# Performance work log

Measured on AMD Instinct MI355X. Metric: run time of the kernel, lower is better.

## Reference

```python
import jax, jax.numpy as jnp
import numpy as np

HIDDEN = 3072
N_HEADS = 24
N_KV = 8
HEAD_DIM = HIDDEN // N_HEADS          # 128
ROT = int(HEAD_DIM * 0.75)            # 96 (partial rotary)
OP_SIZE = N_HEADS * HEAD_DIM + 2 * N_KV * HEAD_DIM  # 5120
LORA_R = 256
LORA_SCALE = 512.0 / LORA_R           # 2.0
ROPE_THETA = 10000.0
SCALE = HEAD_DIM ** -0.5


def setup_inputs() -> dict:
    key = jax.random.key(0)
    ks = jax.random.split(key, 8)
    B, S = 2, 2048
    hidden_states = jax.random.normal(ks[0], (B, S, HIDDEN), dtype=jnp.float32)
    position_ids = jnp.arange(B * S, dtype=jnp.int64 if jax.config.jax_enable_x64 else jnp.int32).reshape(B, S)
    w = lambda k, o, i: jax.random.normal(k, (o, i), dtype=jnp.float32) * (i ** -0.5)
    return {
        "hidden_states": hidden_states,
        "Wqkv": w(ks[1], OP_SIZE, HIDDEN),
        "Aqkv": w(ks[2], LORA_R, HIDDEN),
        "Bqkv": w(ks[3], OP_SIZE, LORA_R) * 0.01,
        "Wo": w(ks[4], HIDDEN, N_HEADS * HEAD_DIM),
        "Ao": w(ks[5], LORA_R, N_HEADS * HEAD_DIM),
        "Bo": w(ks[6], HIDDEN, LORA_R) * 0.01,
        "position_ids": position_ids,
    }


def _lora_linear(x, W, A, Bm):
    # base GEMM + low-rank LoRA update, scaling = alpha/r
    return x @ W.T + (x @ A.T) @ Bm.T * LORA_SCALE


def _rotate_half(x):
    h = x.shape[-1] // 2
    return jnp.concatenate((-x[..., h:], x[..., :h]), axis=-1)


def reference(hidden_states, Wqkv, Aqkv, Bqkv, Wo, Ao, Bo, position_ids):
    B, S, _ = hidden_states.shape
    qkv = _lora_linear(hidden_states, Wqkv, Aqkv, Bqkv)  # [B,S,5120]
    q_pos = N_HEADS * HEAD_DIM
    kv_pos = N_KV * HEAD_DIM
    q = qkv[..., :q_pos].reshape(B, S, N_HEADS, HEAD_DIM)
    k = qkv[..., q_pos:q_pos + kv_pos].reshape(B, S, N_KV, HEAD_DIM)
    v = qkv[..., q_pos + kv_pos:].reshape(B, S, N_KV, HEAD_DIM)

    # partial RoPE: cos/sin cache over rotary_ndims=96
    inv_freq = 1.0 / (ROPE_THETA ** (jnp.arange(0, ROT, 2, dtype=jnp.float32) / ROT))  # [48]
    freqs = position_ids.astype(jnp.float32)[..., None] * inv_freq  # [B,S,48]
    emb = jnp.concatenate((freqs, freqs), axis=-1)                   # [B,S,96]
    cos = jnp.cos(emb)[:, :, None, :]  # broadcast over head axis (bsnd)
    sin = jnp.sin(emb)[:, :, None, :]

    def rope(x):
        xr, xp = x[..., :ROT], x[..., ROT:]
        xr = xr * cos + _rotate_half(xr) * sin
        return jnp.concatenate((xr, xp), axis=-1)

    q = rope(q)
    k = rope(k)

    # GQA: repeat kv heads to match query heads
    groups = N_HEADS // N_KV
    k = jnp.repeat(k, groups, axis=2)
    v = jnp.repeat(v, groups, axis=2)

    scores = jnp.einsum('bqhd,bkhd->bhqk', q, k) * SCALE  # [B,H,S,S]
    causal = jnp.tril(jnp.ones((S, S), dtype=bool))
    scores = jnp.where(causal, scores, jnp.finfo(scores.dtype).min)
    probs = jax.nn.softmax(scores, axis=-1)
    attn = jnp.einsum('bhqk,bkhd->bqhd', probs, v).reshape(B, S, N_HEADS * HEAD_DIM)
    return _lora_linear(attn, Wo, Ao, Bo)
```

## Files before the change

kernel.cpp:

```cpp
#include <hip/hip_runtime.h>

typedef unsigned short u16;
typedef unsigned int   u32;

typedef __bf16 bf16_t;
typedef bf16_t bf16x8 __attribute__((ext_vector_type(8)));
typedef float  f32x4  __attribute__((ext_vector_type(4)));
typedef float  f32x16 __attribute__((ext_vector_type(16)));
typedef u16    u16x8  __attribute__((ext_vector_type(8)));
typedef u32    u32x4  __attribute__((ext_vector_type(4)));

__device__ __forceinline__ float bf2f(u16 u) { return __uint_as_float(((u32)u) << 16); }
__device__ __forceinline__ u16 f2bf(float f) {
  u32 u = __float_as_uint(f);
  u32 r = u + 0x7fffu + ((u >> 16) & 1u);
  return (u16)(r >> 16);
}
__device__ __forceinline__ float fast_exp2(float x) { return __builtin_amdgcn_exp2f(x); }

__device__ __forceinline__ void gload_lds16(const u16* g, u16* l) {
  __builtin_amdgcn_global_load_lds(
      (const __attribute__((address_space(1))) void*)g,
      (__attribute__((address_space(3))) void*)l,
      16, 0, 0);
}

#define SBAR0() __builtin_amdgcn_sched_barrier(0)
#define HWBAR() __builtin_amdgcn_s_barrier()

__global__ void k_cast_all(const float* __restrict__ x,  const float* __restrict__ wq,
                           const float* __restrict__ bq, const float* __restrict__ aq,
                           const float* __restrict__ wo, const float* __restrict__ bo,
                           const float* __restrict__ ao,
                           u16* __restrict__ xw, u16* __restrict__ wwq, u16* __restrict__ aqkvb,
                           u16* __restrict__ wwo, u16* __restrict__ aob) {
  const int total = 5177344;
  int i = blockIdx.x * blockDim.x + threadIdx.x;
  const int stride = gridDim.x * blockDim.x;
  for (; i < total; i += stride) {
    const float* src; u16* dst; int r, c8, L, off, sL;
    if (i < 1572864)      { int loc = i;           r = loc / 384; c8 = loc - r * 384; src = x;  dst = xw;    L = 3328; off = 0;    sL = 3072; }
    else if (i < 3538944) { int loc = i - 1572864; r = loc / 384; c8 = loc - r * 384; src = wq; dst = wwq;   L = 3328; off = 0;    sL = 3072; }
    else if (i < 3702784) { int loc = i - 3538944; r = loc >> 5;  c8 = loc & 31;      src = bq; dst = wwq;   L = 3328; off = 3072; sL = 256;  }
    else if (i < 3801088) { int loc = i - 3702784; r = loc / 384; c8 = loc - r * 384; src = aq; dst = aqkvb; L = 3072; off = 0;    sL = 3072; }
    else if (i < 4980736) { int loc = i - 3801088; r = loc / 384; c8 = loc - r * 384; src = wo; dst = wwo;   L = 3328; off = 0;    sL = 3072; }
    else if (i < 5079040) { int loc = i - 4980736; r = loc >> 5;  c8 = loc & 31;      src = bo; dst = wwo;   L = 3328; off = 3072; sL = 256;  }
    else                  { int loc = i - 5079040; r = loc / 384; c8 = loc - r * 384; src = ao; dst = aob;   L = 3072; off = 0;    sL = 3072; }
    const f32x4* p = (const f32x4*)(src + (size_t)r * sL + c8 * 8);
    f32x4 a = p[0], b2 = p[1];
    u16x8 o;
    o[0] = f2bf(a[0]);  o[1] = f2bf(a[1]);  o[2] = f2bf(a[2]);  o[3] = f2bf(a[3]);
    o[4] = f2bf(b2[0]); o[5] = f2bf(b2[1]); o[6] = f2bf(b2[2]); o[7] = f2bf(b2[3]);
    *(u16x8*)(dst + (size_t)r * L + off + c8 * 8) = o;
  }
}

__global__ void k_red4_cast(const float* __restrict__ t4, u16* __restrict__ out,
                            int C8, int L, int off, float scale, size_t plane) {
  const int r  = blockIdx.y;
  const int c8 = blockIdx.x * 64 + threadIdx.x;
  if (c8 >= C8) return;
  size_t base = (size_t)r * (C8 * 8) + c8 * 8;
  float s[8];
#pragma unroll
  for (int j = 0; j < 8; ++j) s[j] = 0.f;
#pragma unroll
  for (int p = 0; p < 4; ++p) {
    const f32x4* q = (const f32x4*)(t4 + p * plane + base);
    f32x4 a = q[0], b = q[1];
    s[0] += a[0]; s[1] += a[1]; s[2] += a[2]; s[3] += a[3];
    s[4] += b[0]; s[5] += b[1]; s[6] += b[2]; s[7] += b[3];
  }
  u16x8 o;
#pragma unroll
  for (int j = 0; j < 8; ++j) o[j] = f2bf(s[j] * scale);
  *(u16x8*)(out + (size_t)r * L + off + c8 * 8) = o;
}

__global__ __launch_bounds__(256) void k_gemm_bt_sk(
    const u16* __restrict__ A, const u16* __restrict__ B, float* __restrict__ C,
    int M, int N, int lda, int ldb, int kc) {
  __shared__ u16 As[64][64 + 8];
  __shared__ u16 Bs[64][64 + 8];
  const int tid   = threadIdx.x;
  const int lane  = tid & 63;
  const int w     = tid >> 6;
  const int wm    = (w >> 1) * 32;
  const int wn    = (w & 1) * 32;
  const int row16 = lane & 15;
  const int quad  = lane >> 4;
  const int m0 = blockIdx.y * 64;
  const int n0 = blockIdx.x * 64;
  const int ldr = tid >> 2;
  const int ldc = (tid & 3) * 16;
  const int z   = blockIdx.z;
  float* Cz = C + (size_t)z * M * N;
  const int kbeg = z * kc, kend = kbeg + kc;

  f32x4 acc[2][2] = {};

  for (int k0 = kbeg; k0 < kend; k0 += 64) {
    const u16* ga = A + (size_t)(m0 + ldr) * lda + (k0 + ldc);
    const u16* gb = B + (size_t)(n0 + ldr) * ldb + (k0 + ldc);
    u16x8 a0 = *(const u16x8*)ga;
    u16x8 a1 = *(const u16x8*)(ga + 8);
    u16x8 b0 = *(const u16x8*)gb;
    u16x8 b1 = *(const u16x8*)(gb + 8);
    __syncthreads();
    *(u16x8*)&As[ldr][ldc]     = a0;
    *(u16x8*)&As[ldr][ldc + 8] = a1;
    *(u16x8*)&Bs[ldr][ldc]     = b0;
    *(u16x8*)&Bs[ldr][ldc + 8] = b1;
    __syncthreads();
#pragma unroll
    for (int kk = 0; kk < 64; kk += 32) {
      bf16x8 af0 = *(const bf16x8*)&As[wm + row16][kk + quad * 8];
      bf16x8 af1 = *(const bf16x8*)&As[wm + 16 + row16][kk + quad * 8];
      bf16x8 bg0 = *(const bf16x8*)&Bs[wn + row16][kk + quad * 8];
      bf16x8 bg1 = *(const bf16x8*)&Bs[wn + 16 + row16][kk + quad * 8];
      acc[0][0] = __builtin_amdgcn_mfma_f32_16x16x32_bf16(af0, bg0, acc[0][0], 0, 0, 0);
      acc[0][1] = __builtin_amdgcn_mfma_f32_16x16x32_bf16(af0, bg1, acc[0][1], 0, 0, 0);
      acc[1][0] = __builtin_amdgcn_mfma_f32_16x16x32_bf16(af1, bg0, acc[1][0], 0, 0, 0);
      acc[1][1] = __builtin_amdgcn_mfma_f32_16x16x32_bf16(af1, bg1, acc[1][1], 0, 0, 0);
    }
  }
#pragma unroll
  for (int tm = 0; tm < 2; ++tm)
#pragma unroll
    for (int tn = 0; tn < 2; ++tn) {
      int gm = m0 + wm + tm * 16 + quad * 4;
      int gn = n0 + wn + tn * 16 + row16;
#pragma unroll
      for (int r = 0; r < 4; ++r)
        Cz[(size_t)(gm + r) * N + gn] = acc[tm][tn][r];
    }
}

__device__ __forceinline__ void stage_half(
    int H, int nt4,
    const u16* __restrict__ A, const u16* __restrict__ B, int K,
    int m0, int n0, u16* AsB, u16* BsB,
    int w, int rowin, int colsw) {
  if (H >= nt4) return;
  const int t = H >> 2, slot = H & 3;
  const int half = slot & 1;
  const u16* G = (slot < 2) ? A : B;
  const int r0 = (slot < 2) ? m0 : n0;
  u16* lds = ((slot < 2) ? AsB : BsB) + (t & 1) * 16384 + half * 8192;
  const int k0 = t * 64;
#pragma unroll
  for (int i = 0; i < 2; ++i) {
    const int chunk = w * 2 + i;
    const int row = half * 128 + chunk * 8 + rowin;
    gload_lds16(G + (size_t)(r0 + row) * K + k0 + colsw, lds + chunk * 512);
  }
}

__device__ __forceinline__ bf16x8 frag_ld(const u16* base, int row, int c16) {
  return *(const bf16x8*)(base + row * 64 + ((c16 ^ (row & 7)) << 3));
}

template <int RB>
__device__ __forceinline__ void gemm256_group(
    int k, int nt,
    const u16* __restrict__ A, const u16* __restrict__ B, int K,
    int m0, int n0, u16* AsB, u16* BsB,
    int wr, int wc, int row16, int quad, int w, int rowin, int colsw,
    f32x4 (&acc)[8][4]) {
  const u16* Ab = AsB + RB * 16384;
  const u16* Bb = BsB + RB * 16384;
  const int nt4 = nt * 4;
  bf16x8 a0[4][2], a1[4][2], b0[2][2], b1[2][2];

#pragma unroll
  for (int mf = 0; mf < 4; ++mf)
#pragma unroll
    for (int kk = 0; kk < 2; ++kk)
      a0[mf][kk] = frag_ld(Ab, wr * 128 + mf * 16 + row16, kk * 4 + quad);
#pragma unroll
  for (int nf = 0; nf < 2; ++nf)
#pragma unroll
    for (int kk = 0; kk < 2; ++kk)
      b0[nf][kk] = frag_ld(Bb, wc * 64 + nf * 16 + row16, kk * 4 + quad);
  stage_half(4 * k + 5, nt4, A, B, K, m0, n0, AsB, BsB, w, rowin, colsw);
  SBAR0(); HWBAR(); SBAR0();
  __builtin_amdgcn_s_setprio(1);
#pragma unroll
  for (int mf = 0; mf < 4; ++mf)
#pragma unroll
    for (int nf = 0; nf < 2; ++nf)
#pragma unroll
      for (int kk = 0; kk < 2; ++kk)
        acc[mf][nf] = __builtin_amdgcn_mfma_f32_16x16x32_bf16(a0[mf][kk], b0[nf][kk], acc[mf][nf], 0, 0, 0);
  __builtin_amdgcn_s_setprio(0);
  SBAR0(); HWBAR(); SBAR0();

#pragma unroll
  for (int nf = 0; nf < 2; ++nf)
#pragma unroll
    for (int kk = 0; kk < 2; ++kk)
      b1[nf][kk] = frag_ld(Bb, wc * 64 + 32 + nf * 16 + row16, kk * 4 + quad);
  stage_half(4 * k + 6, nt4, A, B, K, m0, n0, AsB, BsB, w, rowin, colsw);
  SBAR0(); HWBAR(); SBAR0();
  __builtin_amdgcn_s_setprio(1);
#pragma unroll
  for (int mf = 0; mf < 4; ++mf)
#pragma unroll
    for (int nf = 0; nf < 2; ++nf)
#pragma unroll
      for (int kk = 0; kk < 2; ++kk)
        acc[mf][2 + nf] = __builtin_amdgcn_mfma_f32_16x16x32_bf16(a0[mf][kk], b1[nf][kk], acc[mf][2 + nf], 0, 0, 0);
  __builtin_amdgcn_s_setprio(0);
  SBAR0(); HWBAR(); SBAR0();

#pragma unroll
  for (int mf = 0; mf < 4; ++mf)
#pragma unroll
    for (int kk = 0; kk < 2; ++kk)
      a1[mf][kk] = frag_ld(Ab, wr * 128 + 64 + mf * 16 + row16, kk * 4 + quad);
  stage_half(4 * k + 7, nt4, A, B, K, m0, n0, AsB, BsB, w, rowin, colsw);
  SBAR0(); HWBAR(); SBAR0();
  __builtin_amdgcn_s_setprio(1);
#pragma unroll
  for (int mf = 0; mf < 4; ++mf)
#pragma unroll
    for (int nf = 0; nf < 2; ++nf)
#pragma unroll
      for (int kk = 0; kk < 2; ++kk)
        acc[4 + mf][nf] = __builtin_amdgcn_mfma_f32_16x16x32_bf16(a1[mf][kk], b0[nf][kk], acc[4 + mf][nf], 0, 0, 0);
  __builtin_amdgcn_s_setprio(0);
  SBAR0(); HWBAR(); SBAR0();

  stage_half(4 * k + 8, nt4, A, B, K, m0, n0, AsB, BsB, w, rowin, colsw);
  SBAR0();
  if (k < nt - 2) { asm volatile("s_waitcnt vmcnt(2)" ::: "memory"); }
  else            { asm volatile("s_waitcnt vmcnt(0)" ::: "memory"); }
  HWBAR(); SBAR0();
  __builtin_amdgcn_s_setprio(1);
#pragma unroll
  for (int mf = 0; mf < 4; ++mf)
#pragma unroll
    for (int nf = 0; nf < 2; ++nf)
#pragma unroll
      for (int kk = 0; kk < 2; ++kk)
        acc[4 + mf][2 + nf] = __builtin_amdgcn_mfma_f32_16x16x32_bf16(a1[mf][kk], b1[nf][kk], acc[4 + mf][2 + nf], 0, 0, 0);
  __builtin_amdgcn_s_setprio(0);
  SBAR0(); HWBAR(); SBAR0();
}

__global__ __launch_bounds__(512, 2) void k_gemm256(
    const u16* __restrict__ A, const u16* __restrict__ B, float* __restrict__ C,
    int M, int N, int K) {
  __shared__ u16 As[2 * 16384];
  __shared__ u16 Bs[2 * 16384];

  const int tid   = threadIdx.x;
  const int lane  = tid & 63;
  const int w     = tid >> 6;
  const int wr    = w >> 2;
  const int wc    = w & 3;
  const int row16 = lane & 15;
  const int quad  = lane >> 4;
  const int rowin = lane >> 3;
  const int colsw = ((lane & 7) ^ (lane >> 3)) << 3;

  const int nwg = (int)gridDim.x;
  const int bid = (int)blockIdx.x;
  const int xcd = bid & 7, rest = bid >> 3;
  const int qq = nwg >> 3, rr = nwg & 7;
  const int wg = (xcd < rr ? xcd * (qq + 1) : rr * (qq + 1) + (xcd - rr) * qq) + rest;
  const int nbx = N >> 8;
  const int m0 = (wg / nbx) << 8;
  const int n0 = (wg % nbx) << 8;

  const int nt = K >> 6;
  f32x4 acc[8][4] = {};

#pragma unroll
  for (int H = 0; H < 5; ++H)
    stage_half(H, nt * 4, A, B, K, m0, n0, As, Bs, w, rowin, colsw);
  asm volatile("s_waitcnt vmcnt(2)" ::: "memory");
  HWBAR(); SBAR0();

  int k = 0;
  for (; k + 1 < nt; k += 2) {
    gemm256_group<0>(k,     nt, A, B, K, m0, n0, As, Bs, wr, wc, row16, quad, w, rowin, colsw, acc);
    gemm256_group<1>(k + 1, nt, A, B, K, m0, n0, As, Bs, wr, wc, row16, quad, w, rowin, colsw, acc);
  }
  if (k < nt)
    gemm256_group<0>(k, nt, A, B, K, m0, n0, As, Bs, wr, wc, row16, quad, w, rowin, colsw, acc);

#pragma unroll
  for (int mi = 0; mi < 8; ++mi) {
    const int gm = m0 + wr * 128 + mi * 16 + quad * 4;
#pragma unroll
    for (int nj = 0; nj < 4; ++nj) {
      const int gn = n0 + wc * 64 + nj * 16 + row16;
#pragma unroll
      for (int r = 0; r < 4; ++r)
        C[(size_t)(gm + r) * N + gn] = acc[mi][nj][r];
    }
  }
}

__global__ void k_rope_tab(const int* __restrict__ pos_ids, float* __restrict__ tab,
                           int* __restrict__ ctr) {
  if (blockIdx.x == 0 && threadIdx.x == 0) *ctr = 0;
  const int t = threadIdx.x;
  const int r = blockIdx.x * 4 + t / 48;
  const int j = t % 48;
  const float pos = (float)pos_ids[r];
  float invf = powf(10000.0f, -(float)j * (1.0f / 48.0f));
  float e = pos * invf;
  tab[(size_t)r * 96 + j]      = cosf(e);
  tab[(size_t)r * 96 + 48 + j] = sinf(e);
}

__global__ void k_rope_v(const float* __restrict__ qkv, const float* __restrict__ tab,
                         u16* __restrict__ qb, u16* __restrict__ kb, u16* __restrict__ vtg) {
  const int y = blockIdx.y;
  const int d = threadIdx.x;
  if (y < 32) {
    const int r  = blockIdx.x;
    const int hh = y;
    const float* src;
    if (hh < 24) src = qkv + (size_t)r * 5120 + hh * 128;
    else         src = qkv + (size_t)r * 5120 + 3072 + (hh - 24) * 128;
    float x = src[d];
    float outv;
    if (d >= 96) {
      outv = x;
    } else {
      int j = (d < 48) ? d : d - 48;
      float c  = tab[(size_t)r * 96 + j];
      float sn = tab[(size_t)r * 96 + 48 + j];
      if (d < 48) outv = x * c - src[d + 48] * sn;
      else        outv = x * c + src[d - 48] * sn;
    }
    u16 o = f2bf(outv);
    if (hh < 24) qb[((size_t)r * 24 + hh) * 128 + d] = o;
    else         kb[((size_t)r * 8 + (hh - 24)) * 128 + d] = o;
  } else {
    const int bk = blockIdx.x >> 8;
    const int kg = blockIdx.x & 255;
    const int b = bk >> 3, kvh = bk & 7;
    const float* src = qkv + (size_t)(b * 2048 + kg * 8) * 5120 + 4096 + kvh * 128 + d;
    u16x8 pack;
#pragma unroll
    for (int t = 0; t < 8; ++t) pack[t] = f2bf(src[(size_t)t * 5120]);
    *(u16x8*)(vtg + ((size_t)bk * 128 + d) * 2048 + kg * 8) = pack;
  }
}

#define NJOBS 768

__global__ __launch_bounds__(256) void k_attn_mfma(
    const u16* __restrict__ qb, const u16* __restrict__ kb, const u16* __restrict__ vtg,
    u16* __restrict__ attnw, int* __restrict__ ctr) {
  __shared__ u16 Ks0[8192], Ks1[8192];
  __shared__ u16 Vt0[8192], Vt1[8192];
  __shared__ int s_job;

  const int tid  = threadIdx.x;
  const int lane = tid & 63;
  const int w    = tid >> 6;
  const int l31  = lane & 31;
  const int hi   = lane >> 5;
  const int r7   = lane & 7;
  const float C1 = 0.08838834764831845f * 1.4426950408889634f;

  for (;;) {
    if (tid == 0) s_job = atomicAdd(ctr, 1);
    __syncthreads();
    const int j = s_job;
    if (j >= NJOBS) return;

    const int qt  = 15 - (j / 48);
    const int bh  = j % 48;
    const int b   = bh / 24;
    const int h   = bh % 24;
    const int kvh = h / 3;
    const int q0  = qt * 128;
    const int qrow = q0 + w * 32 + l31;

    const u16* qrb = qb + (((size_t)(b * 2048 + qrow)) * 24 + h) * 128;
    bf16x8 qf[8];
#pragma unroll
    for (int kk = 0; kk < 8; ++kk) qf[kk] = *(const bf16x8*)(qrb + kk * 16 + hi * 8);

    const u16* kbbase = kb + ((size_t)(b * 2048) * 8 + kvh) * 128;
    const u16* vtbase = vtg + (size_t)(b * 8 + kvh) * 128 * 2048;

    f32x16 o32[4] = {};
    float m_st = -INFINITY, l_st = 0.f;
    const int ntile = 2 * qt + 2;

#define STAGE_K(Kd, KB0)                                                        \
  { _Pragma("unroll") for (int i = 0; i < 4; ++i) {                             \
      const int c = w * 4 + i;                                                  \
      const int rowk = 4 * c + (lane >> 4);                                     \
      gload_lds16(kbbase + (size_t)((KB0) + rowk) * 1024 +                      \
                      (((lane & 15) ^ (rowk & 7)) << 3),                        \
                  (Kd) + c * 512); } }
#define STAGE_V(Vd, KB0)                                                        \
  { _Pragma("unroll") for (int i = 0; i < 4; ++i) {                             \
      const int c = w * 4 + i;                                                  \
      const int rowv = 8 * c + (lane >> 3);                                     \
      gload_lds16(vtbase + (size_t)rowv * 2048 + (KB0) +                        \
                      (((lane & 7) ^ (rowv & 7)) << 3),                         \
                  (Vd) + c * 512); } }

    STAGE_K(Ks0, 0);
    STAGE_V(Vt0, 0);

    for (int t = 0; t < ntile; ++t) {
      const int kb0 = t * 64;
      const u16* Kc = (t & 1) ? Ks1 : Ks0;
      const u16* Vc = (t & 1) ? Vt1 : Vt0;

      asm volatile("s_waitcnt vmcnt(0)" ::: "memory");
      SBAR0(); HWBAR(); SBAR0();
      if (t + 1 < ntile) {
        u16* Kn = (t & 1) ? Ks0 : Ks1;
        u16* Vn = (t & 1) ? Vt0 : Vt1;
        STAGE_K(Kn, kb0 + 64);
        STAGE_V(Vn, kb0 + 64);
      }
      SBAR0();

      f32x16 s0 = {}, s1 = {};
      __builtin_amdgcn_s_setprio(1);
#pragma unroll
      for (int kk = 0; kk < 8; ++kk) {
        bf16x8 kf0 = *(const bf16x8*)&Kc[l31 * 128 + (((2 * kk + hi) ^ r7) << 3)];
        s0 = __builtin_amdgcn_mfma_f32_32x32x16_bf16(kf0, qf[kk], s0, 0, 0, 0);
        bf16x8 kf1 = *(const bf16x8*)&Kc[(32 + l31) * 128 + (((2 * kk + hi) ^ ((32 + l31) & 7)) << 3)];
        s1 = __builtin_amdgcn_mfma_f32_32x32x16_bf16(kf1, qf[kk], s1, 0, 0, 0);
      }
      __builtin_amdgcn_s_setprio(0);

      if (kb0 >= q0) {
#pragma unroll
        for (int r = 0; r < 16; ++r) {
          const int crow = (r & 3) + 8 * (r >> 2) + 4 * hi;
          if (kb0 + crow > qrow)      s0[r] = -INFINITY;
          if (kb0 + 32 + crow > qrow) s1[r] = -INFINITY;
        }
      }

      float tm[8];
#pragma unroll
      for (int r = 0; r < 8; ++r)
        tm[r] = fmaxf(fmaxf(s0[r], s0[r + 8]), fmaxf(s1[r], s1[r + 8]));
#pragma unroll
      for (int st = 4; st >= 1; st >>= 1)
#pragma unroll
        for (int r = 0; r < 4; ++r)
          if (r < st) tm[r] = fmaxf(tm[r], tm[r + st]);
      float mx = fmaxf(tm[0], __shfl_xor(tm[0], 32));

      const bool skip = __all((mx - m_st) * C1 <= 8.0f);
      if (!skip) {
        const float mnew = fmaxf(m_st, mx);
        const float alpha = fast_exp2((m_st - mnew) * C1);
        l_st *= alpha;
#pragma unroll
        for (int dt = 0; dt < 4; ++dt)
#pragma unroll
          for (int r = 0; r < 16; ++r) o32[dt][r] *= alpha;
        m_st = mnew;
      }
      const float mc = m_st * C1;
      float ts[8];
#pragma unroll
      for (int r = 0; r < 16; ++r) {
        s0[r] = fast_exp2(__builtin_fmaf(s0[r], C1, -mc));
        s1[r] = fast_exp2(__builtin_fmaf(s1[r], C1, -mc));
      }
#pragma unroll
      for (int r = 0; r < 8; ++r) ts[r] = (s0[r] + s0[r + 8]) + (s1[r] + s1[r + 8]);
#pragma unroll
      for (int st = 4; st >= 1; st >>= 1)
#pragma unroll
        for (int r = 0; r < 4; ++r)
          if (r < st) ts[r] += ts[r + st];
      l_st += ts[0] + __shfl_xor(ts[0], 32);

#pragma unroll
      for (int kt = 0; kt < 2; ++kt) {
        const f32x16& sv = kt ? s1 : s0;
        u32 pk[8];
#pragma unroll
        for (int i = 0; i < 8; ++i)
          asm("v_cvt_pk_bf16_f32 %0, %1, %2"
              : "=v"(pk[i]) : "v"(sv[2 * i]), "v"(sv[2 * i + 1]));
        u32 e0 = __shfl_xor(hi ? pk[0] : pk[2], 32);
        u32 e1 = __shfl_xor(hi ? pk[1] : pk[3], 32);
        u32 e2 = __shfl_xor(hi ? pk[4] : pk[6], 32);
        u32 e3 = __shfl_xor(hi ? pk[5] : pk[7], 32);
        u32x4 w0, w1;
        w0[0] = hi ? e0 : pk[0]; w0[1] = hi ? e1 : pk[1];
        w0[2] = hi ? pk[2] : e0; w0[3] = hi ? pk[3] : e1;
        w1[0] = hi ? e2 : pk[4]; w1[1] = hi ? e3 : pk[5];
        w1[2] = hi ? pk[6] : e2; w1[3] = hi ? pk[7] : e3;
        bf16x8 pb0 = __builtin_bit_cast(bf16x8, w0);
        bf16x8 pb1 = __builtin_bit_cast(bf16x8, w1);
        __builtin_amdgcn_s_setprio(1);
#pragma unroll
        for (int dt = 0; dt < 4; ++dt) {
          const int vrow = dt * 32 + l31;
          bf16x8 vf0 = *(const bf16x8*)&Vc[vrow * 64 + (((2 * (2 * kt) + hi) ^ (vrow & 7)) << 3)];
          o32[dt] = __builtin_amdgcn_mfma_f32_32x32x16_bf16(vf0, pb0, o32[dt], 0, 0, 0);
          bf16x8 vf1 = *(const bf16x8*)&Vc[vrow * 64 + (((2 * (2 * kt + 1) + hi) ^ (vrow & 7)) << 3)];
          o32[dt] = __builtin_amdgcn_mfma_f32_32x32x16_bf16(vf1, pb1, o32[dt], 0, 0, 0);
        }
        __builtin_amdgcn_s_setprio(0);
      }
    }

    __syncthreads();
    const float inv = 1.0f / l_st;
    u16* scr = ((w < 2) ? Ks0 : Ks1) + (w & 1) * 4096;
#pragma unroll
    for (int dt = 0; dt < 4; ++dt)
#pragma unroll
      for (int r = 0; r < 16; ++r) {
        const int d = 32 * dt + (r & 3) + 8 * (r >> 2) + 4 * hi;
        const int slot = (d >> 3) ^ (l31 & 7);
        scr[l31 * 128 + slot * 8 + (d & 7)] = f2bf(o32[dt][r] * inv);
      }
    const int q32r = lane >> 1, part = lane & 1;
    const size_t grow = ((size_t)(b * 2048 + q0 + w * 32 + q32r)) * 3328 + (size_t)h * 128;
#pragma unroll
    for (int c = 0; c < 8; ++c) {
      const int d0 = part * 64 + c * 8;
      const int s2 = (d0 >> 3) ^ (q32r & 7);
      *(u16x8*)(attnw + grow + d0) = *(const u16x8*)&scr[q32r * 128 + s2 * 8];
    }
  }
}

#define OFF_XW    ((size_t)0)
#define OFF_WWQ   ((size_t)27262976)
#define OFF_AQKVB ((size_t)61341696)
#define OFF_WWO   ((size_t)62914560)
#define OFF_AOB   ((size_t)83361792)
#define OFF_QKV   ((size_t)84934656)
#define OFF_TA4   OFF_QKV
#define OFF_QB    OFF_XW
#define OFF_KB    OFF_WWQ
#define OFF_VTG   (OFF_WWQ + (size_t)8388608)
#define OFF_RTAB  (OFF_WWQ + (size_t)16777216)
#define OFF_CTR   (OFF_WWQ + (size_t)18350080)
#define OFF_ATTNW OFF_QKV
#define OFF_TO4   (OFF_QKV + (size_t)27262976)

extern "C" void kernel_launch(void* const* d_in, const int* in_sizes, int n_in,
                              void* d_out, int out_size, void* d_ws, size_t ws_size,
                              hipStream_t stream) {
  const float* x    = (const float*)d_in[0];
  const float* Wqkv = (const float*)d_in[1];
  const float* Aqkv = (const float*)d_in[2];
  const float* Bqkv = (const float*)d_in[3];
  const float* Wo   = (const float*)d_in[4];
  const float* Ao   = (const float*)d_in[5];
  const float* Bo   = (const float*)d_in[6];
  const int*   pos  = (const int*)d_in[7];
  float* out = (float*)d_out;
  char* ws = (char*)d_ws;

  u16* xw    = (u16*)(ws + OFF_XW);
  u16* wwq   = (u16*)(ws + OFF_WWQ);
  u16* aqkvb = (u16*)(ws + OFF_AQKVB);
  u16* wwo   = (u16*)(ws + OFF_WWO);
  u16* aob   = (u16*)(ws + OFF_AOB);
  float* qkv = (float*)(ws + OFF_QKV);
  float* tA4 = (float*)(ws + OFF_TA4);
  u16* qb    = (u16*)(ws + OFF_QB);
  u16* kb    = (u16*)(ws + OFF_KB);
  u16* vtg   = (u16*)(ws + OFF_VTG);
  float* rtab = (float*)(ws + OFF_RTAB);
  int* ctr   = (int*)(ws + OFF_CTR);
  u16* attnw = (u16*)(ws + OFF_ATTNW);
  float* tO4 = (float*)(ws + OFF_TO4);

  k_cast_all<<<2048, 256, 0, stream>>>(x, Wqkv, Bqkv, Aqkv, Wo, Bo, Ao,
                                       xw, wwq, aqkvb, wwo, aob);

  k_gemm_bt_sk<<<dim3(4, 64, 4), 256, 0, stream>>>(xw, aqkvb, tA4, 4096, 256, 3328, 3072, 768);
  k_red4_cast<<<dim3(1, 4096), 64, 0, stream>>>(tA4, xw, 32, 3328, 3072, 2.f, (size_t)4096 * 256);

  k_gemm256<<<dim3((5120 / 256) * (4096 / 256)), 512, 0, stream>>>(xw, wwq, qkv, 4096, 5120, 3328);

  k_rope_tab<<<dim3(1024), 192, 0, stream>>>(pos, rtab, ctr);
  k_rope_v<<<dim3(4096, 33), 128, 0, stream>>>(qkv, rtab, qb, kb, vtg);

  k_attn_mfma<<<dim3(512), 256, 0, stream>>>(qb, kb, vtg, attnw, ctr);

  k_gemm_bt_sk<<<dim3(4, 64, 4), 256, 0, stream>>>(attnw, aob, tO4, 4096, 256, 3328, 3072, 768);
  k_red4_cast<<<dim3(1, 4096), 64, 0, stream>>>(tO4, attnw, 32, 3328, 3072, 2.f, (size_t)4096 * 256);

  k_gemm256<<<dim3((3072 / 256) * (4096 / 256)), 512, 0, stream>>>(attnw, wwo, out, 4096, 3072, 3328);
}
```

Before: 681.5 us.

## Balance QKV GEMM tiles across CUs with split-K atomic V tiles

The QKV projection GEMM previously launched 320 256x256 tiles, which is more than one wave on 256 CUs. Now 256 blocks each compute one full Q/K tile, and then each computes a quarter-K slice of one V tile, accumulated with atomicAdd into a zeroed buffer. The aim is to remove the second-wave tail imbalance. In exchange it adds a memset, float atomics (non-deterministic summation order), and a separate V output buffer.

```diff
diff --git a/kernel.cpp b/kernel.cpp
--- a/kernel.cpp
+++ b/kernel.cpp
@@ -138,7 +138,7 @@
 
 __device__ __forceinline__ void stage_half(
     int H, int nt4,
-    const u16* __restrict__ A, const u16* __restrict__ B, int K,
+    const u16* __restrict__ A, const u16* __restrict__ B, int S,
     int m0, int n0, u16* AsB, u16* BsB,
     int w, int rowin, int colsw) {
   if (H >= nt4) return;
@@ -152,7 +152,7 @@
   for (int i = 0; i < 2; ++i) {
     const int chunk = w * 2 + i;
     const int row = half * 128 + chunk * 8 + rowin;
-    gload_lds16(G + (size_t)(r0 + row) * K + k0 + colsw, lds + chunk * 512);
+    gload_lds16(G + (size_t)(r0 + row) * S + k0 + colsw, lds + chunk * 512);
   }
 }
 
@@ -163,7 +163,7 @@
 template <int RB>
 __device__ __forceinline__ void gemm256_group(
     int k, int nt,
-    const u16* __restrict__ A, const u16* __restrict__ B, int K,
+    const u16* __restrict__ A, const u16* __restrict__ B, int S,
     int m0, int n0, u16* AsB, u16* BsB,
     int wr, int wc, int row16, int quad, int w, int rowin, int colsw,
     f32x4 (&acc)[8][4]) {
@@ -182,7 +182,7 @@
 #pragma unroll
     for (int kk = 0; kk < 2; ++kk)
       b0[nf][kk] = frag_ld(Bb, wc * 64 + nf * 16 + row16, kk * 4 + quad);
-  stage_half(4 * k + 5, nt4, A, B, K, m0, n0, AsB, BsB, w, rowin, colsw);
+  stage_half(4 * k + 5, nt4, A, B, S, m0, n0, AsB, BsB, w, rowin, colsw);
   SBAR0(); HWBAR(); SBAR0();
   __builtin_amdgcn_s_setprio(1);
 #pragma unroll
@@ -200,7 +200,7 @@
 #pragma unroll
     for (int kk = 0; kk < 2; ++kk)
       b1[nf][kk] = frag_ld(Bb, wc * 64 + 32 + nf * 16 + row16, kk * 4 + quad);
-  stage_half(4 * k + 6, nt4, A, B, K, m0, n0, AsB, BsB, w, rowin, colsw);
+  stage_half(4 * k + 6, nt4, A, B, S, m0, n0, AsB, BsB, w, rowin, colsw);
   SBAR0(); HWBAR(); SBAR0();
   __builtin_amdgcn_s_setprio(1);
 #pragma unroll
@@ -218,7 +218,7 @@
 #pragma unroll
     for (int kk = 0; kk < 2; ++kk)
       a1[mf][kk] = frag_ld(Ab, wr * 128 + 64 + mf * 16 + row16, kk * 4 + quad);
-  stage_half(4 * k + 7, nt4, A, B, K, m0, n0, AsB, BsB, w, rowin, colsw);
+  stage_half(4 * k + 7, nt4, A, B, S, m0, n0, AsB, BsB, w, rowin, colsw);
   SBAR0(); HWBAR(); SBAR0();
   __builtin_amdgcn_s_setprio(1);
 #pragma unroll
@@ -231,7 +231,7 @@
   __builtin_amdgcn_s_setprio(0);
   SBAR0(); HWBAR(); SBAR0();
 
-  stage_half(4 * k + 8, nt4, A, B, K, m0, n0, AsB, BsB, w, rowin, colsw);
+  stage_half(4 * k + 8, nt4, A, B, S, m0, n0, AsB, BsB, w, rowin, colsw);
   SBAR0();
   if (k < nt - 2) { asm volatile("s_waitcnt vmcnt(2)" ::: "memory"); }
   else            { asm volatile("s_waitcnt vmcnt(0)" ::: "memory"); }
@@ -248,12 +248,11 @@
   SBAR0(); HWBAR(); SBAR0();
 }
 
-__global__ __launch_bounds__(512, 2) void k_gemm256(
-    const u16* __restrict__ A, const u16* __restrict__ B, float* __restrict__ C,
-    int M, int N, int K) {
-  __shared__ u16 As[2 * 16384];
-  __shared__ u16 Bs[2 * 16384];
-
+template <int ATOMIC>
+__device__ __forceinline__ void gemm256_run(
+    const u16* __restrict__ A, const u16* __restrict__ B, int S, int nt,
+    int m0, int n0, float* __restrict__ C, int ldc, int cn0,
+    u16* As, u16* Bs) {
   const int tid   = threadIdx.x;
   const int lane  = tid & 63;
   const int w     = tid >> 6;
@@ -264,6 +263,42 @@
   const int rowin = lane >> 3;
   const int colsw = ((lane & 7) ^ (lane >> 3)) << 3;
 
+  f32x4 acc[8][4] = {};
+
+#pragma unroll
+  for (int H = 0; H < 5; ++H)
+    stage_half(H, nt * 4, A, B, S, m0, n0, As, Bs, w, rowin, colsw);
+  asm volatile("s_waitcnt vmcnt(2)" ::: "memory");
+  HWBAR(); SBAR0();
+
+  int k = 0;
+  for (; k + 1 < nt; k += 2) {
+    gemm256_group<0>(k,     nt, A, B, S, m0, n0, As, Bs, wr, wc, row16, quad, w, rowin, colsw, acc);
+    gemm256_group<1>(k + 1, nt, A, B, S, m0, n0, As, Bs, wr, wc, row16, quad, w, rowin, colsw, acc);
+  }
+  if (k < nt)
+    gemm256_group<0>(k, nt, A, B, S, m0, n0, As, Bs, wr, wc, row16, quad, w, rowin, colsw, acc);
+
+#pragma unroll
+  for (int mi = 0; mi < 8; ++mi) {
+    const int gm = m0 + wr * 128 + mi * 16 + quad * 4;
+#pragma unroll
+    for (int nj = 0; nj < 4; ++nj) {
+      const int gn = cn0 + wc * 64 + nj * 16 + row16;
+#pragma unroll
+      for (int r = 0; r < 4; ++r) {
+        if (ATOMIC) atomicAdd(&C[(size_t)(gm + r) * ldc + gn], acc[mi][nj][r]);
+        else        C[(size_t)(gm + r) * ldc + gn] = acc[mi][nj][r];
+      }
+    }
+  }
+}
+
+__global__ __launch_bounds__(512, 2) void k_gemm256(
+    const u16* __restrict__ A, const u16* __restrict__ B, float* __restrict__ C,
+    int M, int N, int K) {
+  __shared__ u16 As[2 * 16384];
+  __shared__ u16 Bs[2 * 16384];
   const int nwg = (int)gridDim.x;
   const int bid = (int)blockIdx.x;
   const int xcd = bid & 7, rest = bid >> 3;
@@ -272,35 +307,27 @@
   const int nbx = N >> 8;
   const int m0 = (wg / nbx) << 8;
   const int n0 = (wg % nbx) << 8;
-
-  const int nt = K >> 6;
-  f32x4 acc[8][4] = {};
-
-#pragma unroll
-  for (int H = 0; H < 5; ++H)
-    stage_half(H, nt * 4, A, B, K, m0, n0, As, Bs, w, rowin, colsw);
-  asm volatile("s_waitcnt vmcnt(2)" ::: "memory");
-  HWBAR(); SBAR0();
-
-  int k = 0;
-  for (; k + 1 < nt; k += 2) {
-    gemm256_group<0>(k,     nt, A, B, K, m0, n0, As, Bs, wr, wc, row16, quad, w, rowin, colsw, acc);
-    gemm256_group<1>(k + 1, nt, A, B, K, m0, n0, As, Bs, wr, wc, row16, quad, w, rowin, colsw, acc);
-  }
-  if (k < nt)
-    gemm256_group<0>(k, nt, A, B, K, m0, n0, As, Bs, wr, wc, row16, quad, w, rowin, colsw, acc);
-
-#pragma unroll
-  for (int mi = 0; mi < 8; ++mi) {
-    const int gm = m0 + wr * 128 + mi * 16 + quad * 4;
-#pragma unroll
-    for (int nj = 0; nj < 4; ++nj) {
-      const int gn = n0 + wc * 64 + nj * 16 + row16;
-#pragma unroll
-      for (int r = 0; r < 4; ++r)
-        C[(size_t)(gm + r) * N + gn] = acc[mi][nj][r];
-    }
-  }
+  gemm256_run<0>(A, B, K, K >> 6, m0, n0, C, N, n0, As, Bs);
+}
+
+__global__ __launch_bounds__(512, 2) void k_gemm256_qkv(
+    const u16* __restrict__ A, const u16* __restrict__ B,
+    float* __restrict__ Cqk, float* __restrict__ Cv) {
+  __shared__ u16 As[2 * 16384];
+  __shared__ u16 Bs[2 * 16384];
+  const int bid = (int)blockIdx.x;
+  const int xcd = bid & 7, rest = bid >> 3;
+  const int wg = xcd * 32 + rest;
+  const int m0 = (wg >> 4) << 8;
+  const int n0 = (wg & 15) << 8;
+  gemm256_run<0>(A, B, 3328, 52, m0, n0, Cqk, 4096, n0, As, Bs);
+  __syncthreads();
+  const int m  = bid & 15;
+  const int nv = (bid >> 4) & 3;
+  const int kc = bid >> 6;
+  const u16* At = A + kc * 832;
+  const u16* Bt = B + (size_t)4096 * 3328 + kc * 832;
+  gemm256_run<1>(At, Bt, 3328, 13, m * 256, nv * 256, Cv, 1024, nv * 256, As, Bs);
 }
 
 __global__ void k_rope_tab(const int* __restrict__ pos_ids, float* __restrict__ tab,
@@ -316,7 +343,8 @@
   tab[(size_t)r * 96 + 48 + j] = sinf(e);
 }
 
-__global__ void k_rope_v(const float* __restrict__ qkv, const float* __restrict__ tab,
+__global__ void k_rope_v(const float* __restrict__ qk, const float* __restrict__ vsrc,
+                         const float* __restrict__ tab,
                          u16* __restrict__ qb, u16* __restrict__ kb, u16* __restrict__ vtg) {
   const int y = blockIdx.y;
   const int d = threadIdx.x;
@@ -324,8 +352,8 @@
     const int r  = blockIdx.x;
     const int hh = y;
     const float* src;
-    if (hh < 24) src = qkv + (size_t)r * 5120 + hh * 128;
-    else         src = qkv + (size_t)r * 5120 + 3072 + (hh - 24) * 128;
+    if (hh < 24) src = qk + (size_t)r * 4096 + hh * 128;
+    else         src = qk + (size_t)r * 4096 + 3072 + (hh - 24) * 128;
     float x = src[d];
     float outv;
     if (d >= 96) {
@@ -344,10 +372,10 @@
     const int bk = blockIdx.x >> 8;
     const int kg = blockIdx.x & 255;
     const int b = bk >> 3, kvh = bk & 7;
-    const float* src = qkv + (size_t)(b * 2048 + kg * 8) * 5120 + 4096 + kvh * 128 + d;
+    const float* src = vsrc + (size_t)(b * 2048 + kg * 8) * 1024 + kvh * 128 + d;
     u16x8 pack;
 #pragma unroll
-    for (int t = 0; t < 8; ++t) pack[t] = f2bf(src[(size_t)t * 5120]);
+    for (int t = 0; t < 8; ++t) pack[t] = f2bf(src[(size_t)t * 1024]);
     *(u16x8*)(vtg + ((size_t)bk * 128 + d) * 2048 + kg * 8) = pack;
   }
 }
@@ -546,6 +574,7 @@
 #define OFF_WWO   ((size_t)62914560)
 #define OFF_AOB   ((size_t)83361792)
 #define OFF_QKV   ((size_t)84934656)
+#define OFF_QKVV  (OFF_QKV + (size_t)67108864)
 #define OFF_TA4   OFF_QKV
 #define OFF_QB    OFF_XW
 #define OFF_KB    OFF_WWQ
@@ -574,7 +603,8 @@
   u16* aqkvb = (u16*)(ws + OFF_AQKVB);
   u16* wwo   = (u16*)(ws + OFF_WWO);
   u16* aob   = (u16*)(ws + OFF_AOB);
-  float* qkv = (float*)(ws + OFF_QKV);
+  float* qk  = (float*)(ws + OFF_QKV);
+  float* qv  = (float*)(ws + OFF_QKVV);
   float* tA4 = (float*)(ws + OFF_TA4);
   u16* qb    = (u16*)(ws + OFF_QB);
   u16* kb    = (u16*)(ws + OFF_KB);
@@ -590,10 +620,11 @@
   k_gemm_bt_sk<<<dim3(4, 64, 4), 256, 0, stream>>>(xw, aqkvb, tA4, 4096, 256, 3328, 3072, 768);
   k_red4_cast<<<dim3(1, 4096), 64, 0, stream>>>(tA4, xw, 32, 3328, 3072, 2.f, (size_t)4096 * 256);
 
-  k_gemm256<<<dim3((5120 / 256) * (4096 / 256)), 512, 0, stream>>>(xw, wwq, qkv, 4096, 5120, 3328);
+  hipMemsetAsync(qv, 0, (size_t)4096 * 1024 * 4, stream);
+  k_gemm256_qkv<<<dim3(256), 512, 0, stream>>>(xw, wwq, qk, qv);
 
   k_rope_tab<<<dim3(1024), 192, 0, stream>>>(pos, rtab, ctr);
-  k_rope_v<<<dim3(4096, 33), 128, 0, stream>>>(qkv, rtab, qb, kb, vtg);
+  k_rope_v<<<dim3(4096, 33), 128, 0, stream>>>(qk, qv, rtab, qb, kb, vtg);
 
   k_attn_mfma<<<dim3(512), 256, 0, stream>>>(qb, kb, vtg, attnw, ctr);
 
```

Result: no change. 684.2 us (+0.4%).
